# Optimization experiments

Measured on AMD Instinct MI355X. Metric: run time of the kernel, lower is better.

Reference implementation:

```python
import jax, jax.numpy as jnp
import numpy as np

D_MODEL, D_STATE, D_CONV, EXPAND = 1024, 16, 4, 2
D_INNER = EXPAND * D_MODEL
B, L = 2, 1024


def setup_inputs() -> dict:
    key = jax.random.key(0)
    ks = jax.random.split(key, 8)
    s = 0.02
    return {
        "x": jax.random.normal(ks[0], (B, L, D_MODEL), jnp.float32),
        "in_proj_w": jax.random.normal(ks[1], (D_MODEL, 2 * D_INNER), jnp.float32) * s,
        "in_proj_b": jnp.zeros((2 * D_INNER,), jnp.float32),
        "conv_w": jax.random.normal(ks[2], (D_INNER, 1, D_CONV), jnp.float32) * s,
        "conv_b": jnp.zeros((D_INNER,), jnp.float32),
        "x_proj_w": jax.random.normal(ks[3], (D_INNER, 2 * D_STATE + D_INNER), jnp.float32) * s,
        "x_proj_b": jnp.zeros((2 * D_STATE + D_INNER,), jnp.float32),
        "dt_proj_w": jax.random.normal(ks[4], (D_STATE, D_INNER), jnp.float32) * s,
        "dt_proj_b": jnp.zeros((D_INNER,), jnp.float32),
        "A_log": jnp.log(jnp.tile(jnp.arange(1, D_STATE + 1, dtype=jnp.float32), (D_INNER, 1))),
        "D": jnp.ones((D_INNER,), jnp.float32),
        "out_proj_w": jax.random.normal(ks[5], (D_INNER, D_MODEL), jnp.float32) * s,
        "out_proj_b": jnp.zeros((D_MODEL,), jnp.float32),
    }


def reference(x, in_proj_w, in_proj_b, conv_w, conv_b, x_proj_w, x_proj_b,
              dt_proj_w, dt_proj_b, A_log, D, out_proj_w, out_proj_b):
    # x: (B, L, d_model)
    xz = x @ in_proj_w + in_proj_b                      # (B, L, 2*d_inner)
    xc, z = jnp.split(xz, 2, axis=-1)
    # causal depthwise conv1d (pad left by d_conv-1 == torch pad then slice [:L])
    xt = jnp.transpose(xc, (0, 2, 1))                   # (B, d_inner, L)
    xt = jax.lax.conv_general_dilated(
        xt, conv_w, window_strides=(1,), padding=[(D_CONV - 1, 0)],
        dimension_numbers=("NCH", "OIH", "NCH"),
        feature_group_count=D_INNER) + conv_b[None, :, None]
    xs = jax.nn.silu(jnp.transpose(xt, (0, 2, 1)))      # (B, L, d_inner)
    proj = xs @ x_proj_w + x_proj_b                     # (B, L, 2*d_state + d_inner)
    dt, Bp, Cp = jnp.split(proj, [D_STATE, 2 * D_STATE], axis=-1)
    # selective scan (log-cumsum parallel form, faithful to source)
    dt = jax.nn.softplus(dt @ dt_proj_w + dt_proj_b)    # (B, L, d_inner)
    A = -jnp.exp(A_log)                                 # (d_inner, d_state)
    dA = jnp.exp(dt[..., None] * A[None, None])         # (B, L, d_inner, d_state)
    dB = dt[..., None] * Bp[:, :, None, :]              # (B, L, d_inner, d_state)
    log_dA = jnp.log(dA + 1e-8)
    prefix = jnp.cumsum(log_dA, axis=1)
    prefix_shift = jnp.pad(prefix[:, :-1], ((0, 0), (1, 0), (0, 0), (0, 0)))
    dBx = dB * xs[..., None]
    h = jnp.cumsum(jnp.exp(prefix_shift) * dBx, axis=1)  # (B, L, d_inner, d_state)
    y = (h * Cp[..., None]).sum(-1)                     # (B, L, d_inner)
    y = y + xs * D
    y = y * jax.nn.silu(z)
    return y @ out_proj_w + out_proj_b                  # (B, L, d_model)
```

## Files before the change

### kernel.cpp

```cpp
#include <hip/hip_runtime.h>

#define DI 2048
#define DM 1024
#define DS 16
#define LEN 1024
#define NB 2
#define NROWS (NB * LEN)
#define NPROJ (2 * DS + DI)
#define NPROJ_PAD 2176
#define N_XZ (2 * DI)
#define CH_R 16
#define NCH (LEN / CH_R)
#define TOTCH (NB * NCH)

using bf16x8 = __attribute__((ext_vector_type(8))) short;
using f32x4  = __attribute__((ext_vector_type(4))) float;

__device__ __forceinline__ unsigned short f32_bf16(float f) {
  unsigned int u = __float_as_uint(f);
  u += 0x7fffu + ((u >> 16) & 1u);
  return (unsigned short)(u >> 16);
}
__device__ __forceinline__ float bf16_f32(unsigned short h) {
  return __uint_as_float((unsigned int)h << 16);
}

__global__ __launch_bounds__(256)
void k_transpose_bf16(const float* __restrict__ W, unsigned short* __restrict__ Wt,
                      int K, int N) {
  __shared__ float tile[32][33];
  const int n0 = blockIdx.x * 32, k0 = blockIdx.y * 32;
  const int tx = threadIdx.x & 31;
  const int ty = threadIdx.x >> 5;
#pragma unroll
  for (int j = 0; j < 32; j += 8) {
    const int n = n0 + tx, k = k0 + ty + j;
    tile[ty + j][tx] = (n < N) ? W[(size_t)k * N + n] : 0.f;
  }
  __syncthreads();
#pragma unroll
  for (int j = 0; j < 32; j += 8)
    Wt[(size_t)(n0 + ty + j) * K + (k0 + tx)] = f32_bf16(tile[tx][ty + j]);
}

__global__ __launch_bounds__(256)
void k_cast_bf16(const float* __restrict__ in, unsigned short* __restrict__ out) {
  const int i8 = (blockIdx.x * 256 + threadIdx.x) * 8;
  const float4 a = *(const float4*)(in + i8);
  const float4 b = *(const float4*)(in + i8 + 4);
  ushort4 lo, hi;
  lo.x = f32_bf16(a.x); lo.y = f32_bf16(a.y); lo.z = f32_bf16(a.z); lo.w = f32_bf16(a.w);
  hi.x = f32_bf16(b.x); hi.y = f32_bf16(b.y); hi.z = f32_bf16(b.z); hi.w = f32_bf16(b.w);
  *(ushort4*)(out + i8) = lo;
  *(ushort4*)(out + i8 + 4) = hi;
}

__global__ __launch_bounds__(512)
void k_gemm_bf(const unsigned short* __restrict__ A, int lda,
               const unsigned short* __restrict__ Bt, int ldb,
               const float* __restrict__ bias,
               float* __restrict__ C, int ldc,
               int K, int Nlog) {
  __shared__ __align__(16) unsigned short As[2][128 * 40];
  __shared__ __align__(16) unsigned short Bs[2][128 * 40];
  const int tid = threadIdx.x;
  const int m0 = blockIdx.y * 128;
  const int n0 = blockIdx.x * 128;
  const int lane = tid & 63;
  const int wid = tid >> 6;
  const int wr = (wid >> 1) * 32;
  const int wc = (wid & 1) * 64;
  const int g = lane >> 4, r = lane & 15;

  const int srow = tid >> 2;
  const int scol = (tid & 3) * 8;

  const unsigned short* Ap = A + (size_t)(m0 + srow) * lda + scol;
  const unsigned short* Bp = Bt + (size_t)(n0 + srow) * ldb + scol;
  const int swoff = srow * 40 + scol;

  f32x4 acc[2][4] = {};
  uint4 ra, rb;

#define LOADG(k0) do {                                                        \
    ra = *(const uint4*)(Ap + (k0));                                          \
    rb = *(const uint4*)(Bp + (k0));                                          \
  } while (0)

#define STORE(bf) do {                                                        \
    *(uint4*)&As[bf][swoff] = ra;                                             \
    *(uint4*)&Bs[bf][swoff] = rb;                                             \
  } while (0)

#define COMPUTE(bf) do {                                                      \
    bf16x8 af[2], bfr[4];                                                     \
    _Pragma("unroll")                                                         \
    for (int i = 0; i < 2; ++i)                                               \
      af[i] = *(const bf16x8*)&As[bf][(wr + i * 16 + r) * 40 + 8 * g];        \
    _Pragma("unroll")                                                         \
    for (int j = 0; j < 4; ++j)                                               \
      bfr[j] = *(const bf16x8*)&Bs[bf][(wc + j * 16 + r) * 40 + 8 * g];       \
    _Pragma("unroll")                                                         \
    for (int i = 0; i < 2; ++i)                                               \
      _Pragma("unroll")                                                       \
      for (int j = 0; j < 4; ++j)                                             \
        acc[i][j] = __builtin_amdgcn_mfma_f32_16x16x32_bf16(af[i], bfr[j],    \
                                                            acc[i][j], 0, 0, 0);\
  } while (0)

  LOADG(0);
  STORE(0);
  __syncthreads();
  int buf = 0;
  for (int k0 = 32; k0 < K; k0 += 32) {
    LOADG(k0);
    COMPUTE(buf);
    STORE(buf ^ 1);
    __syncthreads();
    buf ^= 1;
  }
  COMPUTE(buf);

#undef LOADG
#undef STORE
#undef COMPUTE

#pragma unroll
  for (int i = 0; i < 2; ++i) {
    const int row = m0 + wr + i * 16 + 4 * g;
#pragma unroll
    for (int j = 0; j < 4; ++j) {
      const int col = n0 + wc + j * 16 + r;
      if (col < Nlog) {
        const float bv = bias[col];
#pragma unroll
        for (int q = 0; q < 4; ++q)
          C[(size_t)(row + q) * ldc + col] = acc[i][j][q] + bv;
      }
    }
  }
}

__global__ __launch_bounds__(256)
void k_conv_silu_z(const float* __restrict__ xz, const float* __restrict__ cw,
                   const float* __restrict__ cb,
                   unsigned short* __restrict__ xs, unsigned short* __restrict__ zb) {
  const int idx = blockIdx.x * 256 + threadIdx.x;
  const int d = idx & (DI - 1);
  const int row = idx >> 11;
  const int l = row & (LEN - 1);
  const float w0 = cw[d * 4], w1 = cw[d * 4 + 1], w2 = cw[d * 4 + 2], w3 = cw[d * 4 + 3];
  const float* p = xz + (size_t)row * N_XZ + d;
  float acc = cb[d] + w3 * p[0];
  if (l >= 1) acc += w2 * p[-N_XZ];
  if (l >= 2) acc += w1 * p[-2 * N_XZ];
  if (l >= 3) acc += w0 * p[-3 * N_XZ];
  xs[idx] = f32_bf16(acc / (1.f + expf(-acc)));
  zb[idx] = f32_bf16(p[DI]);
}

__global__ __launch_bounds__(256)
void k_dtproj(const float* __restrict__ proj, const float* __restrict__ w,
              const float* __restrict__ b, float* __restrict__ dt) {
  const int idx = blockIdx.x * 256 + threadIdx.x;
  const int d = idx & (DI - 1);
  const int row = idx >> 11;
  const float* p = proj + (size_t)row * NPROJ;
  float acc = b[d];
#pragma unroll
  for (int s = 0; s < DS; ++s) acc += p[s] * w[s * DI + d];
  dt[idx] = fmaxf(acc, 0.f) + log1pf(expf(-fabsf(acc)));
}

__global__ __launch_bounds__(256)
void k_scanA(const float* __restrict__ dt, const float* __restrict__ proj,
             const unsigned short* __restrict__ xs, const float* __restrict__ Alog,
             float* __restrict__ Ebuf, float* __restrict__ Lbuf) {
  __shared__ float bp_lds[CH_R][DS];
  const int bx = blockIdx.x;
  const int chunkg = bx >> 3;
  const int d = (bx & 7) * 256 + threadIdx.x;
  const int b = chunkg >> 6, c = chunkg & (NCH - 1);
  const int row0 = b * LEN + c * CH_R;
  {
    const int t = threadIdx.x;
    bp_lds[t >> 4][t & 15] = proj[(size_t)(row0 + (t >> 4)) * NPROJ + DS + (t & 15)];
  }
  __syncthreads();

  float a[DS], e[DS], L[DS];
#pragma unroll
  for (int s = 0; s < DS; ++s) {
    a[s] = -expf(Alog[d * DS + s]);
    e[s] = 1.f; L[s] = 0.f;
  }
#pragma unroll 4
  for (int j = 0; j < CH_R; ++j) {
    const size_t row = (size_t)(row0 + j);
    const float dtv = dt[row * DI + d];
    const float xv = bf16_f32(xs[row * DI + d]);
    const float u = dtv * xv;
#pragma unroll
    for (int q = 0; q < 4; ++q) {
      const float4 bq = *(const float4*)&bp_lds[j][q * 4];
      L[q * 4 + 0] += e[q * 4 + 0] * (u * bq.x);
      L[q * 4 + 1] += e[q * 4 + 1] * (u * bq.y);
      L[q * 4 + 2] += e[q * 4 + 2] * (u * bq.z);
      L[q * 4 + 3] += e[q * 4 + 3] * (u * bq.w);
    }
#pragma unroll
    for (int s = 0; s < DS; ++s)
      e[s] *= __expf(dtv * a[s]) + 1e-8f;
  }
  const size_t base = ((size_t)chunkg * DI + d) * DS;
#pragma unroll
  for (int q = 0; q < 4; ++q) {
    *(float4*)&Ebuf[base + q * 4] = make_float4(e[q*4], e[q*4+1], e[q*4+2], e[q*4+3]);
    *(float4*)&Lbuf[base + q * 4] = make_float4(L[q*4], L[q*4+1], L[q*4+2], L[q*4+3]);
  }
}

__global__ __launch_bounds__(256)
void k_scanB(float* __restrict__ Ebuf, float* __restrict__ Lbuf) {
  const int gid = blockIdx.x * 256 + threadIdx.x;
  const int s = gid & 15, d = (gid >> 4) & (DI - 1), b = gid >> 15;
  float scale = 1.f, H = 0.f;
  for (int c = 0; c < NCH; ++c) {
    const size_t idx = (((size_t)(b * NCH + c) * DI + d) << 4) + s;
    const float E = Ebuf[idx], Ls = Lbuf[idx];
    Ebuf[idx] = scale;
    Lbuf[idx] = H;
    H += scale * Ls;
    scale *= E;
  }
}

__global__ __launch_bounds__(256)
void k_scanC(const float* __restrict__ dt, const float* __restrict__ proj,
             const unsigned short* __restrict__ xs, const unsigned short* __restrict__ zb,
             const float* __restrict__ Alog, const float* __restrict__ Dp,
             const float* __restrict__ Ebuf, const float* __restrict__ Lbuf,
             unsigned short* __restrict__ v) {
  __shared__ float bp_lds[CH_R][DS];
  const int bx = blockIdx.x;
  const int chunkg = bx >> 3;
  const int d = (bx & 7) * 256 + threadIdx.x;
  const int b = chunkg >> 6, c = chunkg & (NCH - 1);
  const int row0 = b * LEN + c * CH_R;
  {
    const int t = threadIdx.x;
    bp_lds[t >> 4][t & 15] = proj[(size_t)(row0 + (t >> 4)) * NPROJ + DS + (t & 15)];
  }
  __syncthreads();

  const float Dd = Dp[d];
  float a[DS], e[DS], h[DS];
  const size_t base = ((size_t)chunkg * DI + d) * DS;
#pragma unroll
  for (int q = 0; q < 4; ++q) {
    const float4 ev = *(const float4*)&Ebuf[base + q * 4];
    const float4 hv = *(const float4*)&Lbuf[base + q * 4];
    e[q*4] = ev.x; e[q*4+1] = ev.y; e[q*4+2] = ev.z; e[q*4+3] = ev.w;
    h[q*4] = hv.x; h[q*4+1] = hv.y; h[q*4+2] = hv.z; h[q*4+3] = hv.w;
  }
#pragma unroll
  for (int s = 0; s < DS; ++s)
    a[s] = -expf(Alog[d * DS + s]);

#pragma unroll 4
  for (int j = 0; j < CH_R; ++j) {
    const size_t row = (size_t)(row0 + j);
    const float dtv = dt[row * DI + d];
    const float xv = bf16_f32(xs[row * DI + d]);
    const float u = dtv * xv;
#pragma unroll
    for (int q = 0; q < 4; ++q) {
      const float4 bq = *(const float4*)&bp_lds[j][q * 4];
      h[q * 4 + 0] += e[q * 4 + 0] * (u * bq.x);
      h[q * 4 + 1] += e[q * 4 + 1] * (u * bq.y);
      h[q * 4 + 2] += e[q * 4 + 2] * (u * bq.z);
      h[q * 4 + 3] += e[q * 4 + 3] * (u * bq.w);
    }
    float hs = 0.f;
#pragma unroll
    for (int s = 0; s < DS; ++s) hs += h[s];
    const float cp = proj[row * NPROJ + 2 * DS + d];
    const float z = bf16_f32(zb[row * DI + d]);
    const float y = cp * hs + xv * Dd;
    v[row * DI + d] = f32_bf16(y * (z / (1.f + __expf(-z))));
#pragma unroll
    for (int s = 0; s < DS; ++s)
      e[s] *= __expf(dtv * a[s]) + 1e-8f;
  }
}

extern "C" void kernel_launch(void* const* d_in, const int* in_sizes, int n_in,
                              void* d_out, int out_size, void* d_ws, size_t ws_size,
                              hipStream_t stream) {
  const float* x     = (const float*)d_in[0];
  const float* w_in  = (const float*)d_in[1];
  const float* b_in  = (const float*)d_in[2];
  const float* cw    = (const float*)d_in[3];
  const float* cb    = (const float*)d_in[4];
  const float* w_xp  = (const float*)d_in[5];
  const float* b_xp  = (const float*)d_in[6];
  const float* w_dt  = (const float*)d_in[7];
  const float* b_dt  = (const float*)d_in[8];
  const float* Alog  = (const float*)d_in[9];
  const float* Dp    = (const float*)d_in[10];
  const float* w_out = (const float*)d_in[11];
  const float* b_out = (const float*)d_in[12];
  float* out = (float*)d_out;

  char* ws = (char*)d_ws;
  unsigned short* w1t = (unsigned short*)(ws);
  unsigned short* w2t = (unsigned short*)(ws + 8388608);
  unsigned short* w3t = (unsigned short*)(ws + 17301504);
  unsigned short* xbf = (unsigned short*)(ws + 21495808);
  float* xz   = (float*)(ws + 25690112);
  unsigned short* xsb = (unsigned short*)(ws + 59244544);
  unsigned short* zbf = (unsigned short*)(ws + 67633152);
  float* proj = (float*)(ws + 76021760);
  unsigned short* vb  = (unsigned short*)(ws + 93061120);
  float* dtb  = (float*)(ws);
  float* Ebuf = (float*)(ws + 25690112);
  float* Lbuf = (float*)(ws + 42467328);

  const dim3 blk(256);
  const dim3 blkg(512);
  k_transpose_bf16<<<dim3(4096 / 32, 1024 / 32), blk, 0, stream>>>(w_in, w1t, 1024, 4096);
  k_transpose_bf16<<<dim3(NPROJ_PAD / 32, 2048 / 32), blk, 0, stream>>>(w_xp, w2t, 2048, NPROJ);
  k_transpose_bf16<<<dim3(1024 / 32, 2048 / 32), blk, 0, stream>>>(w_out, w3t, 2048, 1024);
  k_cast_bf16<<<dim3(NROWS * DM / (256 * 8)), blk, 0, stream>>>(x, xbf);
  k_gemm_bf<<<dim3(4096 / 128, 2048 / 128), blkg, 0, stream>>>(xbf, 1024, w1t, 1024, b_in, xz, 4096, 1024, 4096);
  k_conv_silu_z<<<dim3(NROWS * DI / 256), blk, 0, stream>>>(xz, cw, cb, xsb, zbf);
  k_gemm_bf<<<dim3(NPROJ_PAD / 128, 2048 / 128), blkg, 0, stream>>>(xsb, 2048, w2t, 2048, b_xp, proj, NPROJ, 2048, NPROJ);
  k_dtproj<<<dim3(NROWS * DI / 256), blk, 0, stream>>>(proj, w_dt, b_dt, dtb);
  k_scanA<<<dim3(TOTCH * 8), blk, 0, stream>>>(dtb, proj, xsb, Alog, Ebuf, Lbuf);
  k_scanB<<<dim3(NB * DI * DS / 256), blk, 0, stream>>>(Ebuf, Lbuf);
  k_scanC<<<dim3(TOTCH * 8), blk, 0, stream>>>(dtb, proj, xsb, zbf, Alog, Dp, Ebuf, Lbuf, vb);
  k_gemm_bf<<<dim3(1024 / 128, 2048 / 128), blkg, 0, stream>>>(vb, 2048, w3t, 2048, b_out, out, 1024, 2048, 1024);
}
```

Measured before the change: 343.8 us.

## Fuse prep kernels, emit bf16 xz from GEMM, and fold dt projection into scans

Merges the three weight transposes and the input cast into one launch. The first GEMM now writes bf16 output, which removes the fp32 xz buffer and the separate z cast. The dt projection plus softplus is recomputed inside scanA and scanC from LDS-staged weights, so the dt buffer and the dtproj kernel go away. This cuts launches and global memory traffic, but the dt computation is now done twice and LDS use per block goes up.

Result: no change. 337.4 us (-1.9%).

```diff
diff --git a/kernel.cpp b/kernel.cpp
--- a/kernel.cpp
+++ b/kernel.cpp
@@ -25,17 +25,16 @@
   return __uint_as_float((unsigned int)h << 16);
 }
 
-__global__ __launch_bounds__(256)
-void k_transpose_bf16(const float* __restrict__ W, unsigned short* __restrict__ Wt,
-                      int K, int N) {
-  __shared__ float tile[32][33];
-  const int n0 = blockIdx.x * 32, k0 = blockIdx.y * 32;
-  const int tx = threadIdx.x & 31;
-  const int ty = threadIdx.x >> 5;
+__device__ __forceinline__ void transpose_tile(const float* __restrict__ W,
+                                               unsigned short* __restrict__ Wt,
+                                               int K, int N, int bx, int by,
+                                               int tid, float (*tile)[33]) {
+  const int n0 = bx * 32, k0 = by * 32;
+  const int tx = tid & 31, ty = tid >> 5;
 #pragma unroll
   for (int j = 0; j < 32; j += 8) {
-    const int n = n0 + tx, k = k0 + ty + j;
-    tile[ty + j][tx] = (n < N) ? W[(size_t)k * N + n] : 0.f;
+    const int n = n0 + tx;
+    tile[ty + j][tx] = (n < N) ? W[(size_t)(k0 + ty + j) * N + n] : 0.f;
   }
   __syncthreads();
 #pragma unroll
@@ -44,22 +43,40 @@
 }
 
 __global__ __launch_bounds__(256)
-void k_cast_bf16(const float* __restrict__ in, unsigned short* __restrict__ out) {
-  const int i8 = (blockIdx.x * 256 + threadIdx.x) * 8;
-  const float4 a = *(const float4*)(in + i8);
-  const float4 b = *(const float4*)(in + i8 + 4);
-  ushort4 lo, hi;
-  lo.x = f32_bf16(a.x); lo.y = f32_bf16(a.y); lo.z = f32_bf16(a.z); lo.w = f32_bf16(a.w);
-  hi.x = f32_bf16(b.x); hi.y = f32_bf16(b.y); hi.z = f32_bf16(b.z); hi.w = f32_bf16(b.w);
-  *(ushort4*)(out + i8) = lo;
-  *(ushort4*)(out + i8 + 4) = hi;
-}
-
+void k_prep(const float* __restrict__ w_in, const float* __restrict__ w_xp,
+            const float* __restrict__ w_out, const float* __restrict__ x,
+            unsigned short* __restrict__ w1t, unsigned short* __restrict__ w2t,
+            unsigned short* __restrict__ w3t, unsigned short* __restrict__ xbf) {
+  __shared__ float tile[32][33];
+  const int bid = blockIdx.x;
+  const int tid = threadIdx.x;
+  if (bid < 4096) {
+    transpose_tile(w_in, w1t, 1024, 4096, bid % 128, bid / 128, tid, tile);
+  } else if (bid < 8448) {
+    const int b = bid - 4096;
+    transpose_tile(w_xp, w2t, 2048, NPROJ, b % 68, b / 68, tid, tile);
+  } else if (bid < 10496) {
+    const int b = bid - 8448;
+    transpose_tile(w_out, w3t, 2048, 1024, b % 32, b / 32, tid, tile);
+  } else {
+    const int b = bid - 10496;
+    const int i8 = (b * 256 + tid) * 8;
+    const float4 a = *(const float4*)(x + i8);
+    const float4 c = *(const float4*)(x + i8 + 4);
+    ushort4 lo, hi;
+    lo.x = f32_bf16(a.x); lo.y = f32_bf16(a.y); lo.z = f32_bf16(a.z); lo.w = f32_bf16(a.w);
+    hi.x = f32_bf16(c.x); hi.y = f32_bf16(c.y); hi.z = f32_bf16(c.z); hi.w = f32_bf16(c.w);
+    *(ushort4*)(xbf + i8) = lo;
+    *(ushort4*)(xbf + i8 + 4) = hi;
+  }
+}
+
+template <int OUTBF>
 __global__ __launch_bounds__(512)
 void k_gemm_bf(const unsigned short* __restrict__ A, int lda,
                const unsigned short* __restrict__ Bt, int ldb,
                const float* __restrict__ bias,
-               float* __restrict__ C, int ldc,
+               void* __restrict__ Cv, int ldc,
                int K, int Nlog) {
   __shared__ __align__(16) unsigned short As[2][128 * 40];
   __shared__ __align__(16) unsigned short Bs[2][128 * 40];
@@ -133,61 +150,60 @@
       const int col = n0 + wc + j * 16 + r;
       if (col < Nlog) {
         const float bv = bias[col];
-#pragma unroll
-        for (int q = 0; q < 4; ++q)
-          C[(size_t)(row + q) * ldc + col] = acc[i][j][q] + bv;
+        if (OUTBF) {
+          unsigned short* C = (unsigned short*)Cv;
+#pragma unroll
+          for (int q = 0; q < 4; ++q)
+            C[(size_t)(row + q) * ldc + col] = f32_bf16(acc[i][j][q] + bv);
+        } else {
+          float* C = (float*)Cv;
+#pragma unroll
+          for (int q = 0; q < 4; ++q)
+            C[(size_t)(row + q) * ldc + col] = acc[i][j][q] + bv;
+        }
       }
     }
   }
 }
 
 __global__ __launch_bounds__(256)
-void k_conv_silu_z(const float* __restrict__ xz, const float* __restrict__ cw,
-                   const float* __restrict__ cb,
-                   unsigned short* __restrict__ xs, unsigned short* __restrict__ zb) {
+void k_conv_silu(const unsigned short* __restrict__ xzb, const float* __restrict__ cw,
+                 const float* __restrict__ cb, unsigned short* __restrict__ xs) {
   const int idx = blockIdx.x * 256 + threadIdx.x;
   const int d = idx & (DI - 1);
   const int row = idx >> 11;
   const int l = row & (LEN - 1);
   const float w0 = cw[d * 4], w1 = cw[d * 4 + 1], w2 = cw[d * 4 + 2], w3 = cw[d * 4 + 3];
-  const float* p = xz + (size_t)row * N_XZ + d;
-  float acc = cb[d] + w3 * p[0];
-  if (l >= 1) acc += w2 * p[-N_XZ];
-  if (l >= 2) acc += w1 * p[-2 * N_XZ];
-  if (l >= 3) acc += w0 * p[-3 * N_XZ];
+  const unsigned short* p = xzb + (size_t)row * N_XZ + d;
+  float acc = cb[d] + w3 * bf16_f32(p[0]);
+  if (l >= 1) acc += w2 * bf16_f32(p[-N_XZ]);
+  if (l >= 2) acc += w1 * bf16_f32(p[-2 * N_XZ]);
+  if (l >= 3) acc += w0 * bf16_f32(p[-3 * N_XZ]);
   xs[idx] = f32_bf16(acc / (1.f + expf(-acc)));
-  zb[idx] = f32_bf16(p[DI]);
-}
-
-__global__ __launch_bounds__(256)
-void k_dtproj(const float* __restrict__ proj, const float* __restrict__ w,
-              const float* __restrict__ b, float* __restrict__ dt) {
-  const int idx = blockIdx.x * 256 + threadIdx.x;
-  const int d = idx & (DI - 1);
-  const int row = idx >> 11;
-  const float* p = proj + (size_t)row * NPROJ;
-  float acc = b[d];
-#pragma unroll
-  for (int s = 0; s < DS; ++s) acc += p[s] * w[s * DI + d];
-  dt[idx] = fmaxf(acc, 0.f) + log1pf(expf(-fabsf(acc)));
-}
-
-__global__ __launch_bounds__(256)
-void k_scanA(const float* __restrict__ dt, const float* __restrict__ proj,
-             const unsigned short* __restrict__ xs, const float* __restrict__ Alog,
+}
+
+__global__ __launch_bounds__(256)
+void k_scanA(const float* __restrict__ proj, const unsigned short* __restrict__ xs,
+             const float* __restrict__ Alog, const float* __restrict__ w_dt,
+             const float* __restrict__ b_dt,
              float* __restrict__ Ebuf, float* __restrict__ Lbuf) {
   __shared__ float bp_lds[CH_R][DS];
+  __shared__ float dtp_lds[CH_R][DS];
+  __shared__ float wdt_lds[DS][256];
   const int bx = blockIdx.x;
   const int chunkg = bx >> 3;
-  const int d = (bx & 7) * 256 + threadIdx.x;
+  const int t = threadIdx.x;
+  const int d = (bx & 7) * 256 + t;
   const int b = chunkg >> 6, c = chunkg & (NCH - 1);
   const int row0 = b * LEN + c * CH_R;
-  {
-    const int t = threadIdx.x;
-    bp_lds[t >> 4][t & 15] = proj[(size_t)(row0 + (t >> 4)) * NPROJ + DS + (t & 15)];
-  }
+  bp_lds[t >> 4][t & 15] = proj[(size_t)(row0 + (t >> 4)) * NPROJ + DS + (t & 15)];
+  dtp_lds[t >> 4][t & 15] = proj[(size_t)(row0 + (t >> 4)) * NPROJ + (t & 15)];
+#pragma unroll
+  for (int s = 0; s < DS; ++s)
+    wdt_lds[s][t] = w_dt[s * DI + d];
   __syncthreads();
 
+  const float bdt = b_dt[d];
   float a[DS], e[DS], L[DS];
 #pragma unroll
   for (int s = 0; s < DS; ++s) {
@@ -197,7 +213,11 @@
 #pragma unroll 4
   for (int j = 0; j < CH_R; ++j) {
     const size_t row = (size_t)(row0 + j);
-    const float dtv = dt[row * DI + d];
+    float pre = bdt;
+#pragma unroll
+    for (int s = 0; s < DS; ++s)
+      pre += dtp_lds[j][s] * wdt_lds[s][t];
+    const float dtv = fmaxf(pre, 0.f) + log1pf(expf(-fabsf(pre)));
     const float xv = bf16_f32(xs[row * DI + d]);
     const float u = dtv * xv;
 #pragma unroll
@@ -236,23 +256,29 @@
 }
 
 __global__ __launch_bounds__(256)
-void k_scanC(const float* __restrict__ dt, const float* __restrict__ proj,
-             const unsigned short* __restrict__ xs, const unsigned short* __restrict__ zb,
+void k_scanC(const float* __restrict__ proj, const unsigned short* __restrict__ xs,
+             const unsigned short* __restrict__ xzb,
              const float* __restrict__ Alog, const float* __restrict__ Dp,
+             const float* __restrict__ w_dt, const float* __restrict__ b_dt,
              const float* __restrict__ Ebuf, const float* __restrict__ Lbuf,
              unsigned short* __restrict__ v) {
   __shared__ float bp_lds[CH_R][DS];
+  __shared__ float dtp_lds[CH_R][DS];
+  __shared__ float wdt_lds[DS][256];
   const int bx = blockIdx.x;
   const int chunkg = bx >> 3;
-  const int d = (bx & 7) * 256 + threadIdx.x;
+  const int t = threadIdx.x;
+  const int d = (bx & 7) * 256 + t;
   const int b = chunkg >> 6, c = chunkg & (NCH - 1);
   const int row0 = b * LEN + c * CH_R;
-  {
-    const int t = threadIdx.x;
-    bp_lds[t >> 4][t & 15] = proj[(size_t)(row0 + (t >> 4)) * NPROJ + DS + (t & 15)];
-  }
+  bp_lds[t >> 4][t & 15] = proj[(size_t)(row0 + (t >> 4)) * NPROJ + DS + (t & 15)];
+  dtp_lds[t >> 4][t & 15] = proj[(size_t)(row0 + (t >> 4)) * NPROJ + (t & 15)];
+#pragma unroll
+  for (int s = 0; s < DS; ++s)
+    wdt_lds[s][t] = w_dt[s * DI + d];
   __syncthreads();
 
+  const float bdt = b_dt[d];
   const float Dd = Dp[d];
   float a[DS], e[DS], h[DS];
   const size_t base = ((size_t)chunkg * DI + d) * DS;
@@ -270,7 +296,11 @@
 #pragma unroll 4
   for (int j = 0; j < CH_R; ++j) {
     const size_t row = (size_t)(row0 + j);
-    const float dtv = dt[row * DI + d];
+    float pre = bdt;
+#pragma unroll
+    for (int s = 0; s < DS; ++s)
+      pre += dtp_lds[j][s] * wdt_lds[s][t];
+    const float dtv = fmaxf(pre, 0.f) + log1pf(expf(-fabsf(pre)));
     const float xv = bf16_f32(xs[row * DI + d]);
     const float u = dtv * xv;
 #pragma unroll
@@ -285,7 +315,7 @@
 #pragma unroll
     for (int s = 0; s < DS; ++s) hs += h[s];
     const float cp = proj[row * NPROJ + 2 * DS + d];
-    const float z = bf16_f32(zb[row * DI + d]);
+    const float z = bf16_f32(xzb[row * N_XZ + DI + d]);
     const float y = cp * hs + xv * Dd;
     v[row * DI + d] = f32_bf16(y * (z / (1.f + __expf(-z))));
 #pragma unroll
@@ -317,27 +347,21 @@
   unsigned short* w2t = (unsigned short*)(ws + 8388608);
   unsigned short* w3t = (unsigned short*)(ws + 17301504);
   unsigned short* xbf = (unsigned short*)(ws + 21495808);
-  float* xz   = (float*)(ws + 25690112);
-  unsigned short* xsb = (unsigned short*)(ws + 59244544);
-  unsigned short* zbf = (unsigned short*)(ws + 67633152);
-  float* proj = (float*)(ws + 76021760);
-  unsigned short* vb  = (unsigned short*)(ws + 93061120);
-  float* dtb  = (float*)(ws);
-  float* Ebuf = (float*)(ws + 25690112);
-  float* Lbuf = (float*)(ws + 42467328);
+  unsigned short* xzb = (unsigned short*)(ws + 25690112);
+  unsigned short* xsb = (unsigned short*)(ws + 42467328);
+  float* proj = (float*)(ws + 50855936);
+  float* Ebuf = (float*)(ws + 67895296);
+  float* Lbuf = (float*)(ws + 84672512);
+  unsigned short* vb  = (unsigned short*)(ws);
 
   const dim3 blk(256);
   const dim3 blkg(512);
-  k_transpose_bf16<<<dim3(4096 / 32, 1024 / 32), blk, 0, stream>>>(w_in, w1t, 1024, 4096);
-  k_transpose_bf16<<<dim3(NPROJ_PAD / 32, 2048 / 32), blk, 0, stream>>>(w_xp, w2t, 2048, NPROJ);
-  k_transpose_bf16<<<dim3(1024 / 32, 2048 / 32), blk, 0, stream>>>(w_out, w3t, 2048, 1024);
-  k_cast_bf16<<<dim3(NROWS * DM / (256 * 8)), blk, 0, stream>>>(x, xbf);
-  k_gemm_bf<<<dim3(4096 / 128, 2048 / 128), blkg, 0, stream>>>(xbf, 1024, w1t, 1024, b_in, xz, 4096, 1024, 4096);
-  k_conv_silu_z<<<dim3(NROWS * DI / 256), blk, 0, stream>>>(xz, cw, cb, xsb, zbf);
-  k_gemm_bf<<<dim3(NPROJ_PAD / 128, 2048 / 128), blkg, 0, stream>>>(xsb, 2048, w2t, 2048, b_xp, proj, NPROJ, 2048, NPROJ);
-  k_dtproj<<<dim3(NROWS * DI / 256), blk, 0, stream>>>(proj, w_dt, b_dt, dtb);
-  k_scanA<<<dim3(TOTCH * 8), blk, 0, stream>>>(dtb, proj, xsb, Alog, Ebuf, Lbuf);
+  k_prep<<<dim3(11520), blk, 0, stream>>>(w_in, w_xp, w_out, x, w1t, w2t, w3t, xbf);
+  k_gemm_bf<1><<<dim3(4096 / 128, 2048 / 128), blkg, 0, stream>>>(xbf, 1024, w1t, 1024, b_in, xzb, 4096, 1024, 4096);
+  k_conv_silu<<<dim3(NROWS * DI / 256), blk, 0, stream>>>(xzb, cw, cb, xsb);
+  k_gemm_bf<0><<<dim3(NPROJ_PAD / 128, 2048 / 128), blkg, 0, stream>>>(xsb, 2048, w2t, 2048, b_xp, proj, NPROJ, 2048, NPROJ);
+  k_scanA<<<dim3(TOTCH * 8), blk, 0, stream>>>(proj, xsb, Alog, w_dt, b_dt, Ebuf, Lbuf);
   k_scanB<<<dim3(NB * DI * DS / 256), blk, 0, stream>>>(Ebuf, Lbuf);
-  k_scanC<<<dim3(TOTCH * 8), blk, 0, stream>>>(dtb, proj, xsb, zbf, Alog, Dp, Ebuf, Lbuf, vb);
-  k_gemm_bf<<<dim3(1024 / 128, 2048 / 128), blkg, 0, stream>>>(vb, 2048, w3t, 2048, b_out, out, 1024, 2048, 1024);
-}
+  k_scanC<<<dim3(TOTCH * 8), blk, 0, stream>>>(proj, xsb, xzb, Alog, Dp, w_dt, b_dt, Ebuf, Lbuf, vb);
+  k_gemm_bf<0><<<dim3(1024 / 128, 2048 / 128), blkg, 0, stream>>>(vb, 2048, w3t, 2048, b_out, out, 1024, 2048, 1024);
+}
```
